# Optimization experiments

Measured on AMD Instinct MI355X. Metric: run time of the kernel, lower is better.

The kernel has to match this reference:

```python
import jax, jax.numpy as jnp
import numpy as np

H = 2048      # hidden_size
I = 4096      # intermediate_size
N = 128       # ssm state_size
HEADS = 64
P = 64        # head_dim
K = 4         # conv kernel
CHUNK = 256
DT_MIN, DT_MAX = 0.0, 100.0
EPS = 1e-5


def segsum(x):
    # x: (..., T) -> (..., T, T) with out[i, j] = sum_{k=j+1..i} x[k], -inf above diag
    T = x.shape[-1]
    cs = jnp.cumsum(x, axis=-1)
    d = cs[..., :, None] - cs[..., None, :]
    mask = jnp.tril(jnp.ones((T, T), dtype=bool))
    return jnp.where(mask, d, -jnp.inf)


def setup_inputs() -> dict:
    key = jax.random.key(0)
    ks = jax.random.split(key, 8)
    return {
        "hidden_states": jax.random.normal(ks[0], (2, 4096, H), jnp.float32),
        "in_proj_w": jax.random.normal(ks[1], (2 * (I + N) + HEADS, H), jnp.float32) * 0.02,
        "conv_w": jax.random.normal(ks[2], (I + 2 * N, 1, K), jnp.float32) * 0.2,
        "conv_b": jax.random.normal(ks[3], (I + 2 * N,), jnp.float32) * 0.02,
        "dt_bias": jax.random.uniform(ks[4], (HEADS,), jnp.float32),
        "A_log": jnp.log(jax.random.uniform(ks[5], (HEADS,), jnp.float32, 1.0, 16.0)),
        "D": jnp.ones((HEADS,), jnp.float32),
        "norm_w": jnp.ones((I,), jnp.float32),
        "out_proj_w": jax.random.normal(ks[6], (H, I), jnp.float32) * 0.02,
    }


def reference(hidden_states, in_proj_w, conv_w, conv_b, dt_bias, A_log, D, norm_w, out_proj_w):
    b, l, _ = hidden_states.shape
    # in_proj -> [z (I), xBC (I+2N), dt (HEADS)]  (d_mlp == 0 with these dims)
    zxbcdt = hidden_states @ in_proj_w.T
    z, xBC, dt = jnp.split(zxbcdt, [I, I + (I + 2 * N)], axis=-1)

    # causal depthwise conv1d + SiLU
    conv = jax.lax.conv_general_dilated(
        xBC.transpose(0, 2, 1), conv_w, (1,), [(K - 1, 0)],
        dimension_numbers=("NCH", "OIH", "NCH"), feature_group_count=I + 2 * N)
    xBC = jax.nn.silu((conv + conv_b[None, :, None]).transpose(0, 2, 1))
    x, B, C = jnp.split(xBC, [I, I + N], axis=-1)

    A = -jnp.exp(A_log)                                        # (h,)
    dt = jnp.clip(jax.nn.softplus(dt + dt_bias), DT_MIN, DT_MAX)  # (b,l,h)

    # SSD chunked scan (groups = 1 for B/C)
    X = x.reshape(b, l, HEADS, P) * dt[..., None]              # x * dt
    Adt = dt * A                                               # (b,l,h)
    c = l // CHUNK
    Xc = X.reshape(b, c, CHUNK, HEADS, P)
    Bc = B.reshape(b, c, CHUNK, N)
    Cc = C.reshape(b, c, CHUNK, N)
    Ac = Adt.reshape(b, c, CHUNK, HEADS).transpose(0, 3, 1, 2)  # (b,h,c,cl)
    A_cum = jnp.cumsum(Ac, axis=-1)

    # intra-chunk (diagonal) contribution
    L = jnp.exp(segsum(Ac))                                    # (b,h,c,cl,cl)
    Y_diag = jnp.einsum("bcln,bcsn,bhcls,bcshp->bclhp", Cc, Bc, L, Xc)

    # chunk states and inter-chunk recurrence
    decay_states = jnp.exp(A_cum[..., -1:] - A_cum)            # (b,h,c,cl)
    states = jnp.einsum("bcln,bhcl,bclhp->bchpn", Bc, decay_states, Xc)
    states = jnp.concatenate([jnp.zeros_like(states[:, :1]), states], axis=1)
    chunk_A = jnp.pad(A_cum[..., -1], ((0, 0), (0, 0), (1, 0)))  # (b,h,c+1)
    decay_chunk = jnp.exp(segsum(chunk_A))                     # (b,h,c+1,c+1)
    new_states = jnp.einsum("bhzc,bchpn->bzhpn", decay_chunk, states)
    prev_states = new_states[:, :-1]                           # (b,c,h,p,n)

    Y_off = jnp.einsum("bcln,bchpn,bhcl->bclhp", Cc, prev_states, jnp.exp(A_cum))
    y = (Y_diag + Y_off).reshape(b, l, HEADS, P)
    y = y + x.reshape(b, l, HEADS, P) * D[None, None, :, None]  # skip (D term)
    y = y.reshape(b, l, I)

    # gated RMSNorm (norm_before_gate=True): normalize, gate by silu(z), scale
    yf = y.astype(jnp.float32)
    yf = yf * jax.lax.rsqrt(jnp.mean(yf * yf, axis=-1, keepdims=True) + EPS)
    yf = yf * jax.nn.silu(z.astype(jnp.float32))
    y = (norm_w * yf).astype(hidden_states.dtype)

    return y @ out_proj_w.T
```

## Files before the change

### kernel.cpp

```cpp
#include <hip/hip_runtime.h>

typedef unsigned short u16;
typedef __attribute__((ext_vector_type(8))) short bfx8;
typedef __attribute__((ext_vector_type(4))) float f32x4;
typedef __attribute__((ext_vector_type(4))) unsigned short u16x4;

__device__ __forceinline__ float bf2f(u16 u){ return __builtin_bit_cast(float, (unsigned)u << 16); }
__device__ __forceinline__ u16 f2bf(float f){
  unsigned u = __builtin_bit_cast(unsigned, f);
  return (u16)((u + 0x7fffu + ((u >> 16) & 1u)) >> 16);
}

__device__ __forceinline__ void gload_lds16(const void* g, void* l){
  __builtin_amdgcn_global_load_lds((const __attribute__((address_space(1))) void*)g,
                                   (__attribute__((address_space(3))) void*)l, 16, 0, 0);
}

__global__ __launch_bounds__(256) void cvt_kernel(const float* __restrict__ in, u16* __restrict__ out, int n4){
  int i = blockIdx.x * 256 + threadIdx.x;
  if (i >= n4) return;
  f32x4 v = *(const f32x4*)&in[(long)i * 4];
  u16x4 o = { f2bf(v[0]), f2bf(v[1]), f2bf(v[2]), f2bf(v[3]) };
  *(u16x4*)&out[(long)i * 4] = o;
}

__global__ __launch_bounds__(256) void cvt2_kernel(const float* __restrict__ a, u16* __restrict__ oa, int na4,
                                                   const float* __restrict__ b2, u16* __restrict__ ob, int nb4){
  int i = blockIdx.x * 256 + threadIdx.x;
  const float* src; u16* dst; int idx;
  if (i < na4){ src = a; dst = oa; idx = i; }
  else { idx = i - na4; if (idx >= nb4) return; src = b2; dst = ob; }
  f32x4 v = *(const f32x4*)&src[(long)idx * 4];
  u16x4 o = { f2bf(v[0]), f2bf(v[1]), f2bf(v[2]), f2bf(v[3]) };
  *(u16x4*)&dst[(long)idx * 4] = o;
}

template<int F32OUT>
__global__ __launch_bounds__(512, 2)
void gemm256(const u16* __restrict__ A, const u16* __restrict__ W,
             void* __restrict__ out0, void* __restrict__ out1,
             int K, int ld0, int ld1, int nsplit)
{
  __shared__ __align__(16) u16 SA[2][16384];
  __shared__ __align__(16) u16 SB[2][16384];
  const int tid = threadIdx.x;
  const int wid = tid >> 6, lane = tid & 63;
  const int wr = wid >> 2, wc = wid & 3;
  const int bm = blockIdx.x, bn = blockIdx.y;
  const int rr = lane & 15, kg = lane >> 4;
  const int NT = K >> 6;

  const int srow = tid >> 3;
  const int ssw = ((tid & 7) * 16) ^ ((srow & 7) << 4);
  const u16* gA = A + ((long)bm * 256 + srow) * K + (ssw >> 1);
  const u16* gB = W + ((long)bn * 256 + srow) * K + (ssw >> 1);
  const long r64 = (long)64 * K;
  const int dst = tid * 8;

#define STAGE_A(t, ht) { const u16* s_ = gA + (long)(ht) * 2 * r64 + ((t) << 6); \
    gload_lds16(s_,       &SA[(t) & 1][(ht) * 8192 + dst]); \
    gload_lds16(s_ + r64, &SA[(t) & 1][(ht) * 8192 + 4096 + dst]); }
#define STAGE_B(t, ht) { const u16* s_ = gB + (long)(ht) * 2 * r64 + ((t) << 6); \
    gload_lds16(s_,       &SB[(t) & 1][(ht) * 8192 + dst]); \
    gload_lds16(s_ + r64, &SB[(t) & 1][(ht) * 8192 + 4096 + dst]); }

  const int swr = (rr & 7) << 4;
  const int ca0 = ((kg * 16) ^ swr) >> 1;
  const int ca1 = ((64 + kg * 16) ^ swr) >> 1;
  int bA[8], bB[4];
#pragma unroll
  for (int j = 0; j < 8; j++) bA[j] = ((2 * j + wr) * 16 + rr) * 64;
#pragma unroll
  for (int i = 0; i < 4; i++) bB[i] = ((4 * i + wc) * 16 + rr) * 64;

  f32x4 acc[8][4] = {};
  bfx8 af[2][2], bf[4][2];

#define RD_AF(P, F0) { \
    af[0][0] = *(const bfx8*)&SA[P][bA[F0] + ca0];     af[0][1] = *(const bfx8*)&SA[P][bA[F0] + ca1]; \
    af[1][0] = *(const bfx8*)&SA[P][bA[(F0)+1] + ca0]; af[1][1] = *(const bfx8*)&SA[P][bA[(F0)+1] + ca1]; }
#define RD_BF(P) { \
    _Pragma("unroll") \
    for (int i = 0; i < 4; i++){ \
      bf[i][0] = *(const bfx8*)&SB[P][bB[i] + ca0]; bf[i][1] = *(const bfx8*)&SB[P][bB[i] + ca1]; } }
#define PHASE_MFMA(KK) { \
    __builtin_amdgcn_s_setprio(1); \
    _Pragma("unroll") \
    for (int jj = 0; jj < 2; jj++) \
      _Pragma("unroll") \
      for (int i = 0; i < 4; i++){ \
        acc[2*(KK)+jj][i] = __builtin_amdgcn_mfma_f32_16x16x32_bf16(af[jj][0], bf[i][0], acc[2*(KK)+jj][i], 0, 0, 0); \
        acc[2*(KK)+jj][i] = __builtin_amdgcn_mfma_f32_16x16x32_bf16(af[jj][1], bf[i][1], acc[2*(KK)+jj][i], 0, 0, 0); \
      } \
    __builtin_amdgcn_s_setprio(0); }

#define TILE(u, P) { \
     \
    if ((u) + 1 < NT){ STAGE_B((u) + 1, 0); STAGE_B((u) + 1, 1); } \
    asm volatile("s_barrier" ::: "memory"); \
    PHASE_MFMA(0); \
    RD_AF(P, 2); \
     \
    if ((u) + 1 < NT){ STAGE_A((u) + 1, 1); } \
    asm volatile("s_barrier" ::: "memory"); \
    PHASE_MFMA(1); \
    RD_AF(P, 4); \
     \
    asm volatile("s_barrier" ::: "memory"); \
    PHASE_MFMA(2); \
    RD_AF(P, 6); \
     \
    if ((u) + 2 < NT){ STAGE_A((u) + 2, 0); asm volatile("s_waitcnt vmcnt(2)" ::: "memory"); } \
    else if ((u) + 1 < NT){ asm volatile("s_waitcnt vmcnt(0)" ::: "memory"); } \
    asm volatile("s_barrier" ::: "memory"); \
    PHASE_MFMA(3); \
    if ((u) + 1 < NT){ RD_AF((P) ^ 1, 0); RD_BF((P) ^ 1); } \
  }

  STAGE_A(0, 0); STAGE_A(0, 1); STAGE_B(0, 0); STAGE_B(0, 1);
  if (NT > 1) STAGE_A(1, 0);
  asm volatile("s_waitcnt vmcnt(2)" ::: "memory");
  asm volatile("s_barrier" ::: "memory");
  RD_AF(0, 0);
  RD_BF(0);

  for (int uu = 0; uu < NT; uu += 2){
    TILE(uu, 0);
    TILE(uu + 1, 1);
  }
#undef TILE
#undef PHASE_MFMA
#undef RD_BF
#undef RD_AF
#undef STAGE_A
#undef STAGE_B

  int bn2 = bn; void* op = out0; int ldo = ld0;
  if (bn >= nsplit){ bn2 = bn - nsplit; op = out1; ldo = ld1; }
  const int r4b = (lane >> 4) * 4;
#pragma unroll
  for (int j = 0; j < 8; j++)
#pragma unroll
    for (int i = 0; i < 4; i++)
#pragma unroll
      for (int r4 = 0; r4 < 4; r4++){
        long row = (long)bm * 256 + (2 * j + wr) * 16 + r4b + r4;
        long col = (long)bn2 * 256 + (4 * i + wc) * 16 + rr;
        long idx = row * ldo + col;
        if (F32OUT) ((float*)op)[idx] = acc[j][i][r4];
        else        ((u16*)op)[idx]  = f2bf(acc[j][i][r4]);
      }
}

__global__ __launch_bounds__(256) void dt_kernel(const float* __restrict__ hs, const float* __restrict__ w,
                                                 const float* __restrict__ dt_bias, float* __restrict__ dtp){
  __shared__ float hsS[32][66];
  __shared__ float wS[64][66];
  const int tid = threadIdx.x;
  const int j = tid & 63, rgrp = tid >> 6;
  const long row0 = (long)blockIdx.x * 32;
  const int srow = tid >> 3, sc0 = (tid & 7) * 8;
  const int wrow = tid >> 2, wc0 = (tid & 3) * 16;
  const float* hsg = hs + (row0 + srow) * 2048 + sc0;
  const float* wg  = w + (long)(8448 + wrow) * 2048 + wc0;

  f32x4 acc[8] = {};
  for (int k0 = 0; k0 < 2048; k0 += 64){
    *(f32x4*)&hsS[srow][sc0]     = *(const f32x4*)&hsg[k0];
    *(f32x4*)&hsS[srow][sc0 + 4] = *(const f32x4*)&hsg[k0 + 4];
#pragma unroll
    for (int q = 0; q < 4; q++)
      *(f32x4*)&wS[wrow][wc0 + q * 4] = *(const f32x4*)&wg[k0 + q * 4];
    __syncthreads();
#pragma unroll
    for (int kk = 0; kk < 64; kk += 4){
      f32x4 wv = *(const f32x4*)&wS[j][kk];
#pragma unroll
      for (int r = 0; r < 8; r++){
        f32x4 hv = *(const f32x4*)&hsS[rgrp * 8 + r][kk];
        acc[r] += hv * wv;
      }
    }
    __syncthreads();
  }
  float bias = dt_bias[j];
#pragma unroll
  for (int r = 0; r < 8; r++){
    float x = acc[r][0] + acc[r][1] + acc[r][2] + acc[r][3] + bias;
    float sp = (x > 20.f) ? x : log1pf(expf(x));
    sp = fminf(fmaxf(sp, 0.f), 100.f);
    dtp[(row0 + rgrp * 8 + r) * 64 + j] = sp;
  }
}

__global__ __launch_bounds__(64) void acum_kernel(const float* __restrict__ dtp, const float* __restrict__ A_log,
                                                  float* __restrict__ acum, float* __restrict__ suma){
  int bid = blockIdx.x;
  int c = bid & 15, h = (bid >> 4) & 63, b = bid >> 10;
  int lane = threadIdx.x;
  float Ah = -expf(A_log[h]);
  long base = ((long)(b * 4096 + c * 256)) * 64 + h;
  float v[4]; float s = 0.f;
#pragma unroll
  for (int i = 0; i < 4; i++){ float adt = dtp[base + (lane * 4 + i) * 64] * Ah; s += adt; v[i] = s; }
  float tot = s, run = s;
  for (int off = 1; off < 64; off <<= 1){ float u = __shfl_up(run, off); if (lane >= off) run += u; }
  float excl = run - tot;
  long ob = (long)bid * 256 + lane * 4;
#pragma unroll
  for (int i = 0; i < 4; i++) acum[ob + i] = excl + v[i];
  if (lane == 63) suma[bid] = run;
}

__global__ __launch_bounds__(256) void conv_kernel(const u16* __restrict__ xbc, const float* __restrict__ cw,
                                                   const float* __restrict__ cb,
                                                   u16* __restrict__ xact,
                                                   u16* __restrict__ bmat, u16* __restrict__ cmat){
  int pb = blockIdx.x;
  int l0 = (pb & 1023) * 4;
  long pos0 = ((long)(pb >> 10) << 12) + l0;
  for (int cg = threadIdx.x; cg < 544; cg += 256){
    int ch = cg * 8;
    f32x4 cwv[8];
#pragma unroll
    for (int t = 0; t < 8; t++) cwv[t] = *(const f32x4*)&cw[(ch + t) * 4];
    float cbv[8];
#pragma unroll
    for (int t = 0; t < 8; t++) cbv[t] = cb[ch + t];
    bfx8 rr[7];
    bfx8 zz = {};
    rr[0] = (l0 >= 3) ? *(const bfx8*)&xbc[(pos0 - 3) * 4352 + ch] : zz;
    rr[1] = (l0 >= 2) ? *(const bfx8*)&xbc[(pos0 - 2) * 4352 + ch] : zz;
    rr[2] = (l0 >= 1) ? *(const bfx8*)&xbc[(pos0 - 1) * 4352 + ch] : zz;
#pragma unroll
    for (int q = 0; q < 4; q++) rr[3 + q] = *(const bfx8*)&xbc[(pos0 + q) * 4352 + ch];
#pragma unroll
    for (int li = 0; li < 4; li++){
      bfx8 o;
#pragma unroll
      for (int t = 0; t < 8; t++){
        float a = cbv[t] + cwv[t][0] * bf2f((u16)rr[li][t])     + cwv[t][1] * bf2f((u16)rr[li + 1][t])
                         + cwv[t][2] * bf2f((u16)rr[li + 2][t]) + cwv[t][3] * bf2f((u16)rr[li + 3][t]);
        float val = a / (1.f + expf(-a));
        o[t] = (short)f2bf(val);
      }
      long pos = pos0 + li;
      if (ch < 4096)      *(bfx8*)&xact[pos * 4096 + ch] = o;
      else if (ch < 4224) *(bfx8*)&bmat[pos * 128 + ch - 4096] = o;
      else                *(bfx8*)&cmat[pos * 128 + ch - 4224] = o;
    }
  }
}

__global__ __launch_bounds__(256) void bt_transpose(const u16* __restrict__ bmat, u16* __restrict__ bmatT){
  __shared__ u16 T[128 * 136];
  int bx = blockIdx.x;
  int b = bx >> 5, lt = bx & 31;
  int l0 = lt * 128;
  int tid = threadIdx.x;
  for (int idx = tid; idx < 2048; idx += 256){
    int lrow = idx >> 4, ns = (idx & 15) * 8;
    *(bfx8*)&T[lrow * 136 + ns] = *(const bfx8*)&bmat[((long)b * 4096 + l0 + lrow) * 128 + ns];
  }
  __syncthreads();
  for (int idx = tid; idx < 2048; idx += 256){
    int nrow = idx >> 4, ls = (idx & 15) * 8;
    bfx8 o;
#pragma unroll
    for (int j = 0; j < 8; j++) o[j] = (short)T[(ls + j) * 136 + nrow];
    *(bfx8*)&bmatT[(long)b * 524288 + (long)nrow * 4096 + l0 + ls] = o;
  }
}

__global__ __launch_bounds__(256, 4) void states_kernel(const u16* __restrict__ xact, const u16* __restrict__ bmatT,
                                                        const float* __restrict__ acum, const float* __restrict__ suma,
                                                        const float* __restrict__ dtp, u16* __restrict__ stR){
  __shared__ __align__(16) u16 XdT[64 * 264];
  __shared__ float fac[256];
  int bid = blockIdx.x;
  int h = bid & 63, c = (bid >> 6) & 15, b = bid >> 10;
  int tid = threadIdx.x;
  long rowbase = (long)b * 4096 + c * 256;
  long aco = ((long)((b * 64 + h) * 16 + c)) * 256;
  float sA = suma[(b * 64 + h) * 16 + c];
  fac[tid] = dtp[(rowbase + tid) * 64 + h] * expf(sA - acum[aco + tid]);
  __syncthreads();
  for (int idx = tid; idx < 2048; idx += 256){
    int l = idx >> 3, ps = (idx & 7) * 8;
    bfx8 xv = *(const bfx8*)&xact[(rowbase + l) * 4096 + h * 64 + ps];
#pragma unroll
    for (int j = 0; j < 8; j++)
      XdT[(ps + j) * 264 + l] = f2bf(bf2f((u16)xv[j]) * fac[l]);
  }
  __syncthreads();
  int wid = tid >> 6, lane = tid & 63;
  int rr = lane & 15, ko = (lane >> 4) * 8;
  const u16* btb = bmatT + (long)b * 524288 + c * 256;
  f32x4 acc[8] = {};
#pragma unroll
  for (int ks = 0; ks < 8; ks++){
    bfx8 a = *(const bfx8*)&XdT[(wid * 16 + rr) * 264 + ks * 32 + ko];
#pragma unroll
    for (int nt = 0; nt < 8; nt++){
      bfx8 bb = *(const bfx8*)&btb[(long)(nt * 16 + rr) * 4096 + ks * 32 + ko];
      acc[nt] = __builtin_amdgcn_mfma_f32_16x16x32_bf16(a, bb, acc[nt], 0, 0, 0);
    }
  }
  long ob = (long)bid * 8192;
#pragma unroll
  for (int nt = 0; nt < 8; nt++)
#pragma unroll
    for (int r4 = 0; r4 < 4; r4++){
      int p = wid * 16 + (lane >> 4) * 4 + r4;
      stR[ob + p * 128 + nt * 16 + rr] = f2bf(acc[nt][r4]);
    }
}

__global__ __launch_bounds__(256) void scan_kernel(u16* stR, const float* __restrict__ suma){
  int g = blockIdx.x;
  int s = g & 7, bh = g >> 3;
  int b = bh >> 6, h = bh & 63;
  int tid = threadIdx.x;
  long off0 = (long)s * 1024 + tid * 4;
  f32x4 R = {};
  for (int c = 0; c < 16; c++){
    long base = ((long)((b * 16 + c) * 64 + h)) * 8192 + off0;
    float sc = expf(suma[(b * 64 + h) * 16 + c]);
    u16x4 e4 = *(const u16x4*)&stR[base];
    u16x4 o = { f2bf(R[0]), f2bf(R[1]), f2bf(R[2]), f2bf(R[3]) };
    *(u16x4*)&stR[base] = o;
#pragma unroll
    for (int t = 0; t < 4; t++) R[t] = sc * R[t] + bf2f(e4[t]);
  }
}

__global__ __launch_bounds__(256, 3) void ydiag_kernel(const u16* __restrict__ cmat, const u16* __restrict__ bmat,
                                                       const u16* xact,
                                                       const u16* __restrict__ rbuf, const float* __restrict__ acum,
                                                       const float* __restrict__ dtp,
                                                       const float* __restrict__ Dv, u16* ybuf){
  __shared__ __align__(16) u16 XdTq[64 * 72];
  __shared__ __align__(16) u16 Sb[4][64 * 36];
  __shared__ float acL[256];
  __shared__ float dtl[256];
  int bid = blockIdx.x;
  int h = bid & 63, c = (bid >> 6) & 15, b = bid >> 10;
  int tid = threadIdx.x, wid = tid >> 6, lane = tid & 63;
  long rowbase = (long)b * 4096 + c * 256;
  long aco = ((long)((b * 64 + h) * 16 + c)) * 256;
  acL[tid] = acum[aco + tid];
  dtl[tid] = dtp[(rowbase + tid) * 64 + h];
  __syncthreads();

  int rr = lane & 15, ko = (lane >> 4) * 8;
  f32x4 acc[4][4] = {};

  long rb = (long)bid * 8192;
#pragma unroll
  for (int kk = 0; kk < 4; kk++){
    bfx8 cf[4];
#pragma unroll
    for (int lt = 0; lt < 4; lt++)
      cf[lt] = *(const bfx8*)&cmat[(rowbase + wid * 64 + lt * 16 + rr) * 128 + kk * 32 + ko];
#pragma unroll
    for (int pt = 0; pt < 4; pt++){
      bfx8 bb = *(const bfx8*)&rbuf[rb + (pt * 16 + rr) * 128 + kk * 32 + ko];
#pragma unroll
      for (int lt = 0; lt < 4; lt++) acc[lt][pt] = __builtin_amdgcn_mfma_f32_16x16x32_bf16(cf[lt], bb, acc[lt][pt], 0, 0, 0);
    }
  }
#pragma unroll
  for (int lt = 0; lt < 4; lt++)
#pragma unroll
    for (int r4 = 0; r4 < 4; r4++){
      float e = expf(acL[wid * 64 + lt * 16 + (lane >> 4) * 4 + r4]);
#pragma unroll
      for (int pt = 0; pt < 4; pt++) acc[lt][pt][r4] *= e;
    }

  const int nsp = 2 * (wid + 1);
  for (int q = 0; q < 4; q++){
    __syncthreads();
    for (int idx = tid; idx < 512; idx += 256){
      int lq = idx >> 3, ps = (idx & 7) * 8;
      int l = q * 64 + lq;
      bfx8 xv = *(const bfx8*)&xact[(rowbase + l) * 4096 + h * 64 + ps];
#pragma unroll
      for (int j = 0; j < 8; j++)
        XdTq[(ps + j) * 72 + lq] = f2bf(bf2f((u16)xv[j]) * dtl[l]);
    }
    __syncthreads();
#pragma unroll
    for (int sub = 0; sub < 2; sub++){
      int sp = q * 2 + sub;
      if (sp >= nsp) continue;
      int s0 = sp * 32;
      f32x4 sacc[2][4] = {};
#pragma unroll
      for (int kk = 0; kk < 4; kk++){
        bfx8 cf[4];
#pragma unroll
        for (int lt = 0; lt < 4; lt++)
          cf[lt] = *(const bfx8*)&cmat[(rowbase + wid * 64 + lt * 16 + rr) * 128 + kk * 32 + ko];
#pragma unroll
        for (int st = 0; st < 2; st++){
          bfx8 bb = *(const bfx8*)&bmat[(rowbase + s0 + st * 16 + rr) * 128 + kk * 32 + ko];
#pragma unroll
          for (int lt = 0; lt < 4; lt++) sacc[st][lt] = __builtin_amdgcn_mfma_f32_16x16x32_bf16(cf[lt], bb, sacc[st][lt], 0, 0, 0);
        }
      }
#pragma unroll
      for (int st = 0; st < 2; st++)
#pragma unroll
        for (int lt = 0; lt < 4; lt++)
#pragma unroll
          for (int r4 = 0; r4 < 4; r4++){
            int lrow = wid * 64 + lt * 16 + (lane >> 4) * 4 + r4;
            int scol = s0 + st * 16 + rr;
            float vv = (scol <= lrow) ? sacc[st][lt][r4] * expf(acL[lrow] - acL[scol]) : 0.f;
            Sb[wid][(lt * 16 + (lane >> 4) * 4 + r4) * 36 + st * 16 + rr] = f2bf(vv);
          }
      asm volatile("s_waitcnt lgkmcnt(0)" ::: "memory");
      __builtin_amdgcn_sched_barrier(0);
#pragma unroll
      for (int lt = 0; lt < 4; lt++){
        bfx8 a1 = *(const bfx8*)&Sb[wid][(lt * 16 + rr) * 36 + ko];
#pragma unroll
        for (int pt = 0; pt < 4; pt++){
          bfx8 bb = *(const bfx8*)&XdTq[(pt * 16 + rr) * 72 + sub * 32 + ko];
          acc[lt][pt] = __builtin_amdgcn_mfma_f32_16x16x32_bf16(a1, bb, acc[lt][pt], 0, 0, 0);
        }
      }
    }
  }
  float Dh = Dv[h];
#pragma unroll
  for (int lt = 0; lt < 4; lt++)
#pragma unroll
    for (int pt = 0; pt < 4; pt++)
#pragma unroll
      for (int r4 = 0; r4 < 4; r4++){
        int lrow = wid * 64 + lt * 16 + (lane >> 4) * 4 + r4;
        int pcol = pt * 16 + rr;
        long gi = (rowbase + lrow) * 4096 + h * 64 + pcol;
        ybuf[gi] = f2bf(acc[lt][pt][r4] + bf2f(xact[gi]) * Dh);
      }
}

__global__ __launch_bounds__(256) void rms_kernel(const u16* ybuf, const u16* zbuf,
                                                  const float* __restrict__ norm_w, u16* ynorm){
  __shared__ float red[4];
  long row = blockIdx.x;
  int tid = threadIdx.x;
  long yb = row * 4096 + tid * 16;
  bfx8 v0 = *(const bfx8*)&ybuf[yb];
  bfx8 v1 = *(const bfx8*)&ybuf[yb + 8];
  float vals[16];
#pragma unroll
  for (int t = 0; t < 8; t++){ vals[t] = bf2f((u16)v0[t]); vals[8 + t] = bf2f((u16)v1[t]); }
  float ss = 0.f;
#pragma unroll
  for (int t = 0; t < 16; t++) ss += vals[t] * vals[t];
#pragma unroll
  for (int off = 32; off >= 1; off >>= 1) ss += __shfl_xor(ss, off);
  if ((tid & 63) == 0) red[tid >> 6] = ss;
  __syncthreads();
  float rs = rsqrtf((red[0] + red[1] + red[2] + red[3]) * (1.f / 4096.f) + 1e-5f);
  bfx8 z0 = *(const bfx8*)&zbuf[yb];
  bfx8 z1 = *(const bfx8*)&zbuf[yb + 8];
  bfx8 o0, o1;
#pragma unroll
  for (int t = 0; t < 16; t++){
    float zv = bf2f((u16)(t < 8 ? z0[t] : z1[t - 8]));
    float g = zv / (1.f + expf(-zv));
    u16 r = f2bf(vals[t] * rs * norm_w[tid * 16 + t] * g);
    if (t < 8) o0[t] = (short)r; else o1[t - 8] = (short)r;
  }
  *(bfx8*)&ynorm[yb] = o0;
  *(bfx8*)&ynorm[yb + 8] = o1;
}

extern "C" void kernel_launch(void* const* d_in, const int* in_sizes, int n_in,
                              void* d_out, int out_size, void* d_ws, size_t ws_size,
                              hipStream_t stream){
  const float* hs   = (const float*)d_in[0];
  const float* inw  = (const float*)d_in[1];
  const float* cw   = (const float*)d_in[2];
  const float* cb   = (const float*)d_in[3];
  const float* dtb  = (const float*)d_in[4];
  const float* alog = (const float*)d_in[5];
  const float* Dv   = (const float*)d_in[6];
  const float* nw   = (const float*)d_in[7];
  const float* outw = (const float*)d_in[8];

  const size_t REQ = 147857408ULL;
  if (ws_size < REQ){
    hipMemsetAsync(d_out, 0x42, (size_t)out_size * 4, stream);
    return;
  }
  char* ws = (char*)d_ws;
  u16*   hsb  = (u16*)  (ws + 0L);
  u16*   wbi  = (u16*)  (ws + 33554432L);
  u16*   xbc  = (u16*)  (ws + 68157440L);
  u16*   xact = (u16*)  (ws + 0L);
  u16*   stR  = (u16*)  (ws + 68157440L);
  u16*   wbo  = (u16*)  (ws + 101711872L);
  u16*   bmatT= (u16*)  (ws + 118489088L);
  float* dtp  = (float*)(ws + 139460608L);
  float* acum = (float*)(ws + 141557760L);
  float* suma = (float*)(ws + 143654912L);
  u16*   bmat = (u16*)  (ws + 143663104L);
  u16*   cmat = (u16*)  (ws + 145760256L);
  u16*   zbuf = (u16*)  d_out;

  cvt2_kernel<<<33280, 256, 0, stream>>>(hs, hsb, 4194304, inw, wbi, 4325376);
  gemm256<0><<<dim3(32, 33), 512, 0, stream>>>(hsb, wbi, zbuf, xbc, 2048, 4096, 4352, 16);
  dt_kernel<<<256, 256, 0, stream>>>(hs, inw, dtb, dtp);
  acum_kernel<<<2048, 64, 0, stream>>>(dtp, alog, acum, suma);
  conv_kernel<<<2048, 256, 0, stream>>>(xbc, cw, cb, xact, bmat, cmat);
  cvt_kernel<<<8192, 256, 0, stream>>>(outw, wbo, 2097152);
  bt_transpose<<<64, 256, 0, stream>>>(bmat, bmatT);
  states_kernel<<<2048, 256, 0, stream>>>(xact, bmatT, acum, suma, dtp, stR);
  scan_kernel<<<1024, 256, 0, stream>>>(stR, suma);
  ydiag_kernel<<<2048, 256, 0, stream>>>(cmat, bmat, xact, stR, acum, dtp, Dv, xact);
  rms_kernel<<<8192, 256, 0, stream>>>(xact, zbuf, nw, xact);
  gemm256<1><<<dim3(32, 8), 512, 0, stream>>>(xact, wbo, d_out, d_out, 4096, 2048, 2048, 999);
}
```

Measured before the change: 1.017 ms.

## Double-buffer GEMM register fragments and defer B-tile staging in main loop

```diff
diff --git a/kernel.cpp b/kernel.cpp
--- a/kernel.cpp
+++ b/kernel.cpp
@@ -74,61 +74,62 @@
   for (int i = 0; i < 4; i++) bB[i] = ((4 * i + wc) * 16 + rr) * 64;
 
   f32x4 acc[8][4] = {};
-  bfx8 af[2][2], bf[4][2];
-
-#define RD_AF(P, F0) { \
-    af[0][0] = *(const bfx8*)&SA[P][bA[F0] + ca0];     af[0][1] = *(const bfx8*)&SA[P][bA[F0] + ca1]; \
-    af[1][0] = *(const bfx8*)&SA[P][bA[(F0)+1] + ca0]; af[1][1] = *(const bfx8*)&SA[P][bA[(F0)+1] + ca1]; }
-#define RD_BF(P) { \
+  bfx8 afA[2][2], afB[2][2], bfA[4][2], bfB[4][2];
+
+#define RD_AF(DST, P, F0) { \
+    DST[0][0] = *(const bfx8*)&SA[P][bA[F0] + ca0];     DST[0][1] = *(const bfx8*)&SA[P][bA[F0] + ca1]; \
+    DST[1][0] = *(const bfx8*)&SA[P][bA[(F0)+1] + ca0]; DST[1][1] = *(const bfx8*)&SA[P][bA[(F0)+1] + ca1]; }
+#define RD_BF(DST, P) { \
     _Pragma("unroll") \
     for (int i = 0; i < 4; i++){ \
-      bf[i][0] = *(const bfx8*)&SB[P][bB[i] + ca0]; bf[i][1] = *(const bfx8*)&SB[P][bB[i] + ca1]; } }
-#define PHASE_MFMA(KK) { \
+      DST[i][0] = *(const bfx8*)&SB[P][bB[i] + ca0]; DST[i][1] = *(const bfx8*)&SB[P][bB[i] + ca1]; } }
+#define PHASE_MFMA(KK, AF, BF) { \
     __builtin_amdgcn_s_setprio(1); \
     _Pragma("unroll") \
     for (int jj = 0; jj < 2; jj++) \
       _Pragma("unroll") \
       for (int i = 0; i < 4; i++){ \
-        acc[2*(KK)+jj][i] = __builtin_amdgcn_mfma_f32_16x16x32_bf16(af[jj][0], bf[i][0], acc[2*(KK)+jj][i], 0, 0, 0); \
-        acc[2*(KK)+jj][i] = __builtin_amdgcn_mfma_f32_16x16x32_bf16(af[jj][1], bf[i][1], acc[2*(KK)+jj][i], 0, 0, 0); \
+        acc[2*(KK)+jj][i] = __builtin_amdgcn_mfma_f32_16x16x32_bf16(AF[jj][0], BF[i][0], acc[2*(KK)+jj][i], 0, 0, 0); \
+        acc[2*(KK)+jj][i] = __builtin_amdgcn_mfma_f32_16x16x32_bf16(AF[jj][1], BF[i][1], acc[2*(KK)+jj][i], 0, 0, 0); \
       } \
     __builtin_amdgcn_s_setprio(0); }
-
-#define TILE(u, P) { \
+#define LGKM_BAR { asm volatile("s_waitcnt lgkmcnt(0)" ::: "memory"); asm volatile("s_barrier" ::: "memory"); }
+
+#define TILE(u, P, BFC, BFN) { \
      \
-    if ((u) + 1 < NT){ STAGE_B((u) + 1, 0); STAGE_B((u) + 1, 1); } \
-    asm volatile("s_barrier" ::: "memory"); \
-    PHASE_MFMA(0); \
-    RD_AF(P, 2); \
+    LGKM_BAR; \
+    PHASE_MFMA(0, afA, BFC); \
+    RD_AF(afB, P, 2); \
      \
-    if ((u) + 1 < NT){ STAGE_A((u) + 1, 1); } \
-    asm volatile("s_barrier" ::: "memory"); \
-    PHASE_MFMA(1); \
-    RD_AF(P, 4); \
+    if ((u) + 1 < NT){ STAGE_B((u) + 1, 0); STAGE_B((u) + 1, 1); STAGE_A((u) + 1, 1); } \
+    LGKM_BAR; \
+    PHASE_MFMA(1, afB, BFC); \
+    RD_AF(afA, P, 4); \
      \
-    asm volatile("s_barrier" ::: "memory"); \
-    PHASE_MFMA(2); \
-    RD_AF(P, 6); \
+    LGKM_BAR; \
+    PHASE_MFMA(2, afA, BFC); \
+    RD_AF(afB, P, 6); \
      \
-    if ((u) + 2 < NT){ STAGE_A((u) + 2, 0); asm volatile("s_waitcnt vmcnt(2)" ::: "memory"); } \
-    else if ((u) + 1 < NT){ asm volatile("s_waitcnt vmcnt(0)" ::: "memory"); } \
-    asm volatile("s_barrier" ::: "memory"); \
-    PHASE_MFMA(3); \
-    if ((u) + 1 < NT){ RD_AF((P) ^ 1, 0); RD_BF((P) ^ 1); } \
+    if ((u) + 2 < NT)      { STAGE_A((u) + 2, 0); asm volatile("s_waitcnt vmcnt(2)" ::: "memory"); } \
+    else if ((u) + 1 < NT) { asm volatile("s_waitcnt vmcnt(0)" ::: "memory"); } \
+    LGKM_BAR; \
+    PHASE_MFMA(3, afB, BFC); \
+    if ((u) + 1 < NT){ RD_AF(afA, (P) ^ 1, 0); RD_BF(BFN, (P) ^ 1); } \
   }
 
   STAGE_A(0, 0); STAGE_A(0, 1); STAGE_B(0, 0); STAGE_B(0, 1);
   if (NT > 1) STAGE_A(1, 0);
   asm volatile("s_waitcnt vmcnt(2)" ::: "memory");
   asm volatile("s_barrier" ::: "memory");
-  RD_AF(0, 0);
-  RD_BF(0);
+  RD_AF(afA, 0, 0);
+  RD_BF(bfA, 0);
 
   for (int uu = 0; uu < NT; uu += 2){
-    TILE(uu, 0);
-    TILE(uu + 1, 1);
+    TILE(uu, 0, bfA, bfB);
+    TILE(uu + 1, 1, bfB, bfA);
   }
 #undef TILE
+#undef LGKM_BAR
 #undef PHASE_MFMA
 #undef RD_BF
 #undef RD_AF
```

New measurement: 1.100 ms. 1.08x slower.
